# Kernel optimization log

Hardware: AMD Instinct MI355X
Metric: run time of the kernel (lower is better)

The kernel has to match this reference:

```python
import jax, jax.numpy as jnp
import numpy as np

HEADS = 16

def setup_inputs() -> dict:
    key = jax.random.key(0)
    ks = jax.random.split(key, 5)
    B, T, D = 2, 2048, 2048
    s = 0.02
    return {
        "x": jax.random.normal(ks[0], (B, T, D), dtype=jnp.float32),
        "Wq": jax.random.normal(ks[1], (D, D), dtype=jnp.float32) * s,
        "Wk": jax.random.normal(ks[2], (D, D), dtype=jnp.float32) * s,
        "Wv": jax.random.normal(ks[3], (D, D), dtype=jnp.float32) * s,
        "Wo": jax.random.normal(ks[4], (D, D), dtype=jnp.float32) * s,
    }

def reference(x, Wq, Wk, Wv, Wo):
    B, T, _ = x.shape
    H = HEADS
    Dh = Wq.shape[1] // H
    # projections: [B,T,H,Dh]
    q = (x @ Wq).reshape(B, T, H, Dh)
    k = (x @ Wk).reshape(B, T, H, Dh)
    v = (x @ Wv).reshape(B, T, H, Dh)
    # raw scores [B,H,T,T]
    scores = jnp.einsum("bthd,bshd->bhts", q, k)
    # NOTE (faithful to source): mask is multiplicative 0/1 tril (the
    # masked_fill(-inf) in the torch code is not in-place and has no effect),
    # and the scale is sqrt(token_len), not sqrt(head_dim).
    mask = jnp.tril(jnp.ones((T, T), dtype=scores.dtype))
    scores = scores * mask
    attn = jax.nn.softmax(scores / (T ** 0.5), axis=-1)
    out = jnp.einsum("bhts,bshd->bthd", attn, v).reshape(B, T, H * Dh)
    return out @ Wo
```

## Files before the change

### kernel.cpp

```cpp
#include <hip/hip_runtime.h>


typedef __attribute__((ext_vector_type(4))) float  f32x4;
typedef __attribute__((ext_vector_type(8))) short  bf16x8;
typedef __attribute__((ext_vector_type(4))) unsigned short u16x4;

#define AS1 __attribute__((address_space(1)))
#define AS3 __attribute__((address_space(3)))

__device__ __forceinline__ void llds16(const void* g, void* l) {
  __builtin_amdgcn_global_load_lds((const AS1 void*)g, (AS3 void*)l, 16, 0, 0);
}

__device__ __forceinline__ unsigned short f2bf(float f) {
  unsigned int u = __builtin_bit_cast(unsigned int, f);
  u += 0x7fffu + ((u >> 16) & 1u);
  return (unsigned short)(u >> 16);
}

__device__ __forceinline__ unsigned short f2bfru(float f) {
  return (unsigned short)((__builtin_bit_cast(unsigned int, f) + 0x8000u) >> 16);
}

__device__ __forceinline__ float bf2f(unsigned short u) {
  return __builtin_bit_cast(float, (unsigned int)u << 16);
}

__global__ __launch_bounds__(256) void cast_x_kernel(const float* __restrict__ in,
                                                     unsigned short* __restrict__ out) {
  int i = blockIdx.x * 256 + threadIdx.x;
  f32x4 v = ((const f32x4*)in)[i];
  u16x4 o;
  o[0] = f2bf(v[0]); o[1] = f2bf(v[1]); o[2] = f2bf(v[2]); o[3] = f2bf(v[3]);
  ((u16x4*)out)[i] = o;
}

__global__ __launch_bounds__(256) void transpose_w4_kernel(
    const float* __restrict__ W0, const float* __restrict__ W1,
    const float* __restrict__ W2, const float* __restrict__ W3,
    unsigned short* __restrict__ T0, unsigned short* __restrict__ T1,
    unsigned short* __restrict__ T2, unsigned short* __restrict__ T3) {
  __shared__ float tile[32][33];
  const int z = blockIdx.z;
  const float* W = (z == 0) ? W0 : (z == 1) ? W1 : (z == 2) ? W2 : W3;
  unsigned short* Wt = (z == 0) ? T0 : (z == 1) ? T1 : (z == 2) ? T2 : T3;
  const int bx = blockIdx.x << 5;
  const int by = blockIdx.y << 5;
  const int tx = threadIdx.x;
  const int ty = threadIdx.y;
#pragma unroll
  for (int r = ty; r < 32; r += 8)
    tile[r][tx] = W[(size_t)(bx + r) * 2048 + by + tx];
  __syncthreads();
#pragma unroll
  for (int r = ty; r < 32; r += 8)
    Wt[(size_t)(by + r) * 2048 + bx + tx] = f2bf(tile[tx][r]);
}

__global__ __launch_bounds__(512, 2) void gemm_qkv(const unsigned short* __restrict__ A,
                                                   const unsigned short* __restrict__ Bt,
                                                   unsigned short* __restrict__ Qb,
                                                   unsigned short* __restrict__ Kb,
                                                   unsigned short* __restrict__ Vt) {
  constexpr int SLOT = 49152;
  __shared__ __align__(16) char smem[3 * SLOT];
  const int tid  = threadIdx.x;
  const int lane = tid & 63;
  const int w    = tid >> 6;
  const int wr   = w >> 2;
  const int wc   = w & 3;
  const int q16  = lane >> 4;
  const int l15  = lane & 15;
  const int f    = blockIdx.x;
  const int g    = f >> 3;
  const int bn   = (f & 7) * 3 + (g % 3);
  const int bm   = g / 3;

  const int srow = tid >> 3;
  const int scl  = (tid & 7) ^ (srow & 7);
  const unsigned short* aS = A  + (size_t)((bm << 7) + srow) * 2048 + (scl << 3);
  const unsigned short* bS = Bt + (size_t)(bn * 256 + srow) * 2048 + (scl << 3);
  const int sdst = tid << 4;

  const int swzb = (q16 ^ (l15 & 7)) << 4;
  const int aRd  = ((wr << 6) + l15) << 7;
  const int bRd  = 16384 + ((wc << 6) + l15) << 7 == 0 ? 0 : 16384 + (((wc << 6) + l15) << 7);

  f32x4 acc[4][4];
#pragma unroll
  for (int i = 0; i < 4; ++i)
#pragma unroll
    for (int j = 0; j < 4; ++j) acc[i][j] = (f32x4){0.f, 0.f, 0.f, 0.f};

  auto stageT = [&](int kt, char* sb) {
    const size_t ko = (size_t)kt << 6;
    llds16(aS + ko,              sb + sdst);
    llds16(aS + (64 * 2048) + ko, sb + 8192 + sdst);
#pragma unroll
    for (int r = 0; r < 4; ++r)
      llds16(bS + (size_t)r * (64 * 2048) + ko, sb + 16384 + (r << 13) + sdst);
  };

  auto computeT = [&](const char* base) {
#pragma unroll
    for (int ks = 0; ks < 2; ++ks) {
      const int sw = swzb ^ (ks << 6);
      bf16x8 af[4], bf[4];
#pragma unroll
      for (int mi = 0; mi < 4; ++mi)
        af[mi] = *(const bf16x8*)(base + aRd + (mi << 11) + sw);
#pragma unroll
      for (int ni = 0; ni < 4; ++ni)
        bf[ni] = *(const bf16x8*)(base + 16384 + (((wc << 6) + l15) << 7) + (ni << 11) + sw);
      __builtin_amdgcn_s_setprio(1);
#pragma unroll
      for (int mi = 0; mi < 4; ++mi)
#pragma unroll
        for (int ni = 0; ni < 4; ++ni)
          acc[mi][ni] = __builtin_amdgcn_mfma_f32_16x16x32_bf16(af[mi], bf[ni], acc[mi][ni], 0, 0, 0);
      __builtin_amdgcn_s_setprio(0);
    }
  };

  char* s0 = smem;
  char* s1 = smem + SLOT;
  char* s2 = smem + 2 * SLOT;

#define W6()  asm volatile("s_waitcnt vmcnt(6)" ::: "memory")
#define W0()  asm volatile("s_waitcnt vmcnt(0)" ::: "memory")
#define BAR() __builtin_amdgcn_s_barrier()

  stageT(0, s0); stageT(1, s1);
  W6(); BAR();
  stageT(2, s2);
  computeT(s0);
#pragma unroll 1
  for (int b = 1; b <= 25; b += 3) {
    W6(); BAR(); stageT(b + 2, s0); computeT(s1);
    W6(); BAR(); stageT(b + 3, s1); computeT(s2);
    W6(); BAR(); stageT(b + 4, s2); computeT(s0);
  }
  W6(); BAR(); stageT(30, s0); computeT(s1);
  W6(); BAR(); stageT(31, s1); computeT(s2);
  W6(); BAR(); computeT(s0);
  W0(); BAR(); computeT(s1);

#undef W6
#undef W0
#undef BAR

  const float qscale = 0.02209708691207961f;
  const int rb = q16 << 2;
#pragma unroll
  for (int mi = 0; mi < 4; ++mi) {
    int m0 = (bm << 7) + (wr << 6) + (mi << 4) + rb;
#pragma unroll
    for (int ni = 0; ni < 4; ++ni) {
      int gn = (bn << 8) + (wc << 6) + (ni << 4) + l15;
      int region = gn >> 11;
      int nloc = gn & 2047;
      if (region == 0) {
#pragma unroll
        for (int j = 0; j < 4; ++j)
          Qb[(size_t)(m0 + j) * 2048 + nloc] = f2bf(acc[mi][ni][j] * qscale);
      } else if (region == 1) {
#pragma unroll
        for (int j = 0; j < 4; ++j)
          Kb[(size_t)(m0 + j) * 2048 + nloc] = f2bf(acc[mi][ni][j]);
      } else {
        u16x4 pk;
#pragma unroll
        for (int j = 0; j < 4; ++j) pk[j] = f2bf(acc[mi][ni][j]);
        int b = m0 >> 11, t = m0 & 2047;
        *(u16x4*)(Vt + ((size_t)((b << 4) + (nloc >> 7)) * 128 + (nloc & 127)) * 2048 + t) = pk;
      }
    }
  }
}

__global__ __launch_bounds__(256, 2) void gemm_wo(const unsigned short* __restrict__ A,
                                                  const unsigned short* __restrict__ Bt,
                                                  float* __restrict__ Co) {
  constexpr int SLOT = 8192 + 8192;
  __shared__ __align__(16) char smem[3 * SLOT];

  const int tid  = threadIdx.x;
  const int lane = tid & 63;
  const int w    = tid >> 6;
  const int q16  = lane >> 4;
  const int l15  = lane & 15;
  const int f    = blockIdx.x;
  const int g    = f >> 3;
  const int bn   = ((f & 7) << 1) + (g & 1);
  const int bm   = g >> 1;
  const int wmb  = (w >> 1) << 6;
  const int wnb  = (w & 1) << 6;

  f32x4 acc[4][4];
#pragma unroll
  for (int i = 0; i < 4; ++i)
#pragma unroll
    for (int j = 0; j < 4; ++j) acc[i][j] = (f32x4){0.f, 0.f, 0.f, 0.f};

  const int rowA = tid >> 2;
  const int chA  = tid & 3;
  auto stageT = [&](int t, char* sb) {
    const int k0 = t << 5;
#pragma unroll
    for (int r = 0; r < 2; ++r) {
      int row = (r << 6) + rowA;
      const unsigned short* src = A + (size_t)((bm << 7) + row) * 2048 + k0
                                    + ((chA ^ ((row >> 1) & 3)) << 3);
      llds16(src, sb + (r << 12) + (w << 10));
    }
#pragma unroll
    for (int r = 0; r < 2; ++r) {
      int row = (r << 6) + rowA;
      const unsigned short* src = Bt + (size_t)((bn << 7) + row) * 2048 + k0
                                     + ((chA ^ ((row >> 1) & 3)) << 3);
      llds16(src, sb + 8192 + (r << 12) + (w << 10));
    }
  };

  auto computeT = [&](const char* base) {
    bf16x8 af[4], bf[4];
#pragma unroll
    for (int mi = 0; mi < 4; ++mi) {
      int row = wmb + (mi << 4) + l15;
      af[mi] = *(const bf16x8*)(base + (row << 6) + ((q16 ^ ((row >> 1) & 3)) << 4));
    }
#pragma unroll
    for (int ni = 0; ni < 4; ++ni) {
      int row = wnb + (ni << 4) + l15;
      bf[ni] = *(const bf16x8*)(base + 8192 + (row << 6) + ((q16 ^ ((row >> 1) & 3)) << 4));
    }
    __builtin_amdgcn_s_setprio(1);
#pragma unroll
    for (int mi = 0; mi < 4; ++mi)
#pragma unroll
      for (int ni = 0; ni < 4; ++ni)
        acc[mi][ni] = __builtin_amdgcn_mfma_f32_16x16x32_bf16(af[mi], bf[ni], acc[mi][ni], 0, 0, 0);
    __builtin_amdgcn_s_setprio(0);
  };

  auto STEP = [&](int t, char* cbase, char* sbase) {
    asm volatile("s_waitcnt vmcnt(4)" ::: "memory");
    __builtin_amdgcn_s_barrier();
    stageT(t + 2, sbase);
    computeT(cbase);
  };

  char* s0 = smem;
  char* s1 = smem + SLOT;
  char* s2 = smem + 2 * SLOT;

  stageT(0, s0); stageT(1, s1);
#pragma unroll 1
  for (int t = 0; t < 60; t += 3) {
    STEP(t,     s0, s2);
    STEP(t + 1, s1, s0);
    STEP(t + 2, s2, s1);
  }
  STEP(60, s0, s2);
  STEP(61, s1, s0);
  asm volatile("s_waitcnt vmcnt(4)" ::: "memory");
  __builtin_amdgcn_s_barrier();
  computeT(s2);
  asm volatile("s_waitcnt vmcnt(0)" ::: "memory");
  __builtin_amdgcn_s_barrier();
  computeT(s0);

  const int rb = q16 << 2;
#pragma unroll
  for (int mi = 0; mi < 4; ++mi) {
    int m0 = (bm << 7) + wmb + (mi << 4) + rb;
#pragma unroll
    for (int ni = 0; ni < 4; ++ni) {
      int n = (bn << 7) + wnb + (ni << 4) + l15;
#pragma unroll
      for (int j = 0; j < 4; ++j)
        Co[(size_t)(m0 + j) * 2048 + n] = acc[mi][ni][j];
    }
  }
}

__global__ __launch_bounds__(256) void vsuf_kernel(const unsigned short* __restrict__ Vt,
                                                   float* __restrict__ Suf) {
  const int row  = blockIdx.x * 4 + (threadIdx.x >> 6);
  const int lane = threadIdx.x & 63;
  const unsigned short* vp = Vt + (size_t)row * 2048 + (lane << 5);
  float a = 0.f;
#pragma unroll
  for (int c = 0; c < 4; ++c) {
    bf16x8 v = *(const bf16x8*)(vp + (c << 3));
#pragma unroll
    for (int j = 0; j < 8; ++j) a += bf2f((unsigned short)v[j]);
  }
  float I = a;
#pragma unroll
  for (int off = 1; off < 64; off <<= 1) {
    float t = __shfl_down(I, off, 64);
    I += (lane + off < 64) ? t : 0.f;
  }
  Suf[(size_t)lane * 4096 + row] = I;
  if (lane == 0) Suf[(size_t)64 * 4096 + row] = 0.f;
}

__global__ __launch_bounds__(256) void attn_kernel(const unsigned short* __restrict__ Q,
                                                   const unsigned short* __restrict__ K,
                                                   const unsigned short* __restrict__ V,
                                                   const float* __restrict__ Suf,
                                                   unsigned short* __restrict__ O) {
  __shared__ __align__(16) char smem[36864];
  const int tid  = threadIdx.x;
  const int lane = tid & 63;
  const int w    = tid >> 6;
  const int q16  = lane >> 4;
  const int l15  = lane & 15;
  const int f    = blockIdx.x;
  const int bh    = ((f & 7) << 2) + ((f >> 3) & 3);
  const int strip = 31 - (f >> 5);
  const int b  = bh >> 4;
  const size_t qkbase = ((size_t)(b << 11)) * 2048 + ((size_t)(bh & 15) << 7);
  const size_t vbase  = (size_t)bh << 18;
  const int rb = q16 << 2;
  char* Psm = smem + 32768 + (w << 10);

  const int numIter = 2 * strip + 2;
  const int t0 = (strip << 6) + (w << 4);

  auto stage = [&](int s0, int kb, int vb) {
#pragma unroll
    for (int c = 0; c < 2; ++c) {
      int ch = (w << 1) + c;
      int rowK = (ch << 2) + q16;
      int colbK = (l15 << 4) ^ ((rowK & 7) << 4);
      llds16(K + qkbase + (size_t)(s0 + rowK) * 2048 + (colbK >> 1), smem + kb + (ch << 10));
      int rowV = (ch << 4) + (lane >> 2);
      int colbV = ((lane & 3) << 4) ^ (((rowV >> 2) & 3) << 4);
      llds16(V + vbase + (size_t)rowV * 2048 + s0 + (colbV >> 1), smem + vb + (ch << 10));
    }
  };

  bf16x8 qf[4];
  {
    const unsigned short* qp = Q + qkbase + (size_t)(t0 + l15) * 2048 + (q16 << 3);
#pragma unroll
    for (int kk = 0; kk < 4; ++kk) qf[kk] = *(const bf16x8*)(qp + (kk << 5));
  }

  f32x4 oacc[8];
#pragma unroll
  for (int i = 0; i < 8; ++i) oacc[i] = (f32x4){0.f, 0.f, 0.f, 0.f};
  float ell[4] = {0.f, 0.f, 0.f, 0.f};

  stage(0, 0, 16384);
  asm volatile("s_waitcnt vmcnt(0)" ::: "memory");
  __syncthreads();

  int cur = 0;
  for (int it = 0; it < numIter; ++it) {
    const int s0 = it << 5;
    if (it + 1 < numIter)
      stage(s0 + 32, (cur ^ 1) << 13, 16384 + ((cur ^ 1) << 13));

    if (s0 <= t0) {
      const int kb = cur << 13;
      const int vb = 16384 + (cur << 13);

      f32x4 sA = (f32x4){0.f, 0.f, 0.f, 0.f}, sB = (f32x4){0.f, 0.f, 0.f, 0.f};
#pragma unroll
      for (int kk = 0; kk < 4; ++kk) {
        int r0 = l15;
        bf16x8 k0f = *(const bf16x8*)(smem + kb + (r0 << 8) + (((kk << 6) + (q16 << 4)) ^ ((r0 & 7) << 4)));
        sA = __builtin_amdgcn_mfma_f32_16x16x32_bf16(qf[kk], k0f, sA, 0, 0, 0);
        int r1 = 16 + l15;
        bf16x8 k1f = *(const bf16x8*)(smem + kb + (r1 << 8) + (((kk << 6) + (q16 << 4)) ^ ((r1 & 7) << 4)));
        sB = __builtin_amdgcn_mfma_f32_16x16x32_bf16(qf[kk], k1f, sB, 0, 0, 0);
      }

      float pA[4], pB[4];
      if (s0 + 31 <= t0) {
#pragma unroll
        for (int j = 0; j < 4; ++j) {
          pA[j] = __expf(sA[j]);
          pB[j] = __expf(sB[j]);
          ell[j] += pA[j] + pB[j];
        }
      } else {
#pragma unroll
        for (int j = 0; j < 4; ++j) {
          int t  = t0 + rb + j;
          int sa = s0 + l15;
          float vA = (sa <= t)      ? sA[j] : 0.f;
          float vB = (sa + 16 <= t) ? sB[j] : 0.f;
          pA[j] = __expf(vA);
          pB[j] = __expf(vB);
          ell[j] += pA[j] + pB[j];
        }
      }

#pragma unroll
      for (int j = 0; j < 4; ++j) {
        int r   = rb + j;
        int swz = ((r >> 1) & 3) << 4;
        *(unsigned short*)(Psm + (r << 6) + ((l15 << 1) ^ swz))        = f2bfru(pA[j]);
        *(unsigned short*)(Psm + (r << 6) + ((32 + (l15 << 1)) ^ swz)) = f2bfru(pB[j]);
      }
      asm volatile("s_waitcnt lgkmcnt(0)" ::: "memory");

      bf16x8 pa;
      {
        int r = l15;
        pa = *(const bf16x8*)(Psm + (r << 6) + ((q16 << 4) ^ (((r >> 1) & 3) << 4)));
      }
#pragma unroll
      for (int ni = 0; ni < 8; ++ni) {
        int dr = (ni << 4) + l15;
        bf16x8 vbf = *(const bf16x8*)(smem + vb + (dr << 6) + ((q16 << 4) ^ (((dr >> 2) & 3) << 4)));
        oacc[ni] = __builtin_amdgcn_mfma_f32_16x16x32_bf16(pa, vbf, oacc[ni], 0, 0, 0);
      }
    }

    asm volatile("s_waitcnt vmcnt(0)" ::: "memory");
    __syncthreads();
    cur ^= 1;
  }

  const int send = (t0 & ~31) + 32;
  const float* sp = Suf + (size_t)(send >> 5) * 4096 + ((size_t)bh << 7);
  const float extra = (float)(2048 - send);
#pragma unroll
  for (int ni = 0; ni < 8; ++ni) {
    float sv = sp[(ni << 4) + l15];
#pragma unroll
    for (int j = 0; j < 4; ++j) oacc[ni][j] += sv;
  }

#pragma unroll
  for (int j = 0; j < 4; ++j) {
    float r = ell[j];
    r += __shfl_xor(r, 1, 64);
    r += __shfl_xor(r, 2, 64);
    r += __shfl_xor(r, 4, 64);
    r += __shfl_xor(r, 8, 64);
    float inv = 1.0f / (r + extra);
    int t = t0 + rb + j;
    unsigned short* op = O + qkbase + (size_t)t * 2048;
#pragma unroll
    for (int ni = 0; ni < 8; ++ni)
      op[(ni << 4) + l15] = f2bf(oacc[ni][j] * inv);
  }
}

extern "C" void kernel_launch(void* const* d_in, const int* in_sizes, int n_in,
                              void* d_out, int out_size, void* d_ws, size_t ws_size,
                              hipStream_t stream) {
  (void)in_sizes; (void)n_in; (void)out_size; (void)ws_size;
  const float* x  = (const float*)d_in[0];
  const float* Wq = (const float*)d_in[1];
  const float* Wk = (const float*)d_in[2];
  const float* Wv = (const float*)d_in[3];
  const float* Wo = (const float*)d_in[4];
  float* out = (float*)d_out;

  char* ws = (char*)d_ws;
  unsigned short* Xb  = (unsigned short*)(ws);
  unsigned short* Wqt = (unsigned short*)(ws + 16777216);
  unsigned short* Wkt = (unsigned short*)(ws + 16777216 + 8388608);
  unsigned short* Wvt = (unsigned short*)(ws + 16777216 + 2 * 8388608);
  unsigned short* Wot = (unsigned short*)(ws + 16777216 + 3 * 8388608);
  unsigned short* Qb  = (unsigned short*)(ws + 50331648);
  unsigned short* Kb  = (unsigned short*)(ws + 67108864);
  unsigned short* Vt  = (unsigned short*)(ws + 83886080);
  unsigned short* Ob  = Xb;
  float*          Suf = (float*)Wqt;

  cast_x_kernel<<<8192, 256, 0, stream>>>(x, Xb);
  {
    dim3 tb(32, 8), tg(64, 64, 4);
    transpose_w4_kernel<<<tg, tb, 0, stream>>>(Wq, Wk, Wv, Wo, Wqt, Wkt, Wvt, Wot);
  }
  gemm_qkv<<<768, 512, 0, stream>>>(Xb, Wqt, Qb, Kb, Vt);

  vsuf_kernel<<<1024, 256, 0, stream>>>(Vt, Suf);

  attn_kernel<<<1024, 256, 0, stream>>>(Qb, Kb, Vt, Suf, Ob);

  gemm_wo<<<512, 256, 0, stream>>>(Ob, Wot, out);
}
```

Measured before the change: 265.7 us.

## Retile QKV GEMM to 128x384 tiles with BK=32 and 512 blocks

Replaces the 128x256 tile, BK=64 QKV projection GEMM with a 128x384 tile and BK=32 K-step, so each warp computes a 64x96 sub-tile (4x6 MFMA accumulators). The grid drops from 768 to 512 blocks, which fits exactly two waves of 256 CUs at two blocks per CU. Each block reuses its A loads across more output columns and uses less LDS per stage. The cost is twice as many K iterations and barriers, plus more accumulator registers per thread.

```diff
diff --git a/kernel.cpp b/kernel.cpp
--- a/kernel.cpp
+++ b/kernel.cpp
@@ -57,12 +57,12 @@
     Wt[(size_t)(by + r) * 2048 + bx + tx] = f2bf(tile[tx][r]);
 }
 
-__global__ __launch_bounds__(512, 2) void gemm_qkv(const unsigned short* __restrict__ A,
-                                                   const unsigned short* __restrict__ Bt,
-                                                   unsigned short* __restrict__ Qb,
-                                                   unsigned short* __restrict__ Kb,
-                                                   unsigned short* __restrict__ Vt) {
-  constexpr int SLOT = 49152;
+__global__ __launch_bounds__(512, 2) void gemm_qkv2(const unsigned short* __restrict__ A,
+                                                    const unsigned short* __restrict__ Bt,
+                                                    unsigned short* __restrict__ Qb,
+                                                    unsigned short* __restrict__ Kb,
+                                                    unsigned short* __restrict__ Vt) {
+  constexpr int SLOT = 32768;
   __shared__ __align__(16) char smem[3 * SLOT];
   const int tid  = threadIdx.x;
   const int lane = tid & 63;
@@ -72,81 +72,73 @@
   const int q16  = lane >> 4;
   const int l15  = lane & 15;
   const int f    = blockIdx.x;
-  const int g    = f >> 3;
-  const int bn   = (f & 7) * 3 + (g % 3);
-  const int bm   = g / 3;
-
-  const int srow = tid >> 3;
-  const int scl  = (tid & 7) ^ (srow & 7);
+  const int bn   = ((f & 7) << 1) + ((f >> 3) & 1);
+  const int bm   = f >> 4;
+
+  const int srow = tid >> 2;
+  const int scl  = (tid & 3) ^ ((srow >> 1) & 3);
   const unsigned short* aS = A  + (size_t)((bm << 7) + srow) * 2048 + (scl << 3);
-  const unsigned short* bS = Bt + (size_t)(bn * 256 + srow) * 2048 + (scl << 3);
+  const unsigned short* bS = Bt + (size_t)(bn * 384 + srow) * 2048 + (scl << 3);
   const int sdst = tid << 4;
 
-  const int swzb = (q16 ^ (l15 & 7)) << 4;
-  const int aRd  = ((wr << 6) + l15) << 7;
-  const int bRd  = 16384 + ((wc << 6) + l15) << 7 == 0 ? 0 : 16384 + (((wc << 6) + l15) << 7);
-
-  f32x4 acc[4][4];
+  const int swx   = (q16 ^ ((l15 >> 1) & 3)) << 4;
+  const int aBase = (((wr << 6) + l15) << 6) + swx;
+  const int bBase = 8192 + ((wc * 96 + l15) << 6) + swx;
+
+  f32x4 acc[4][6];
 #pragma unroll
   for (int i = 0; i < 4; ++i)
 #pragma unroll
-    for (int j = 0; j < 4; ++j) acc[i][j] = (f32x4){0.f, 0.f, 0.f, 0.f};
+    for (int j = 0; j < 6; ++j) acc[i][j] = (f32x4){0.f, 0.f, 0.f, 0.f};
 
   auto stageT = [&](int kt, char* sb) {
-    const size_t ko = (size_t)kt << 6;
-    llds16(aS + ko,              sb + sdst);
-    llds16(aS + (64 * 2048) + ko, sb + 8192 + sdst);
-#pragma unroll
-    for (int r = 0; r < 4; ++r)
-      llds16(bS + (size_t)r * (64 * 2048) + ko, sb + 16384 + (r << 13) + sdst);
+    const size_t ko = (size_t)kt << 5;
+    llds16(aS + ko, sb + sdst);
+#pragma unroll
+    for (int r = 0; r < 3; ++r)
+      llds16(bS + (size_t)r * (128 * 2048) + ko, sb + 8192 + (r << 13) + sdst);
   };
 
   auto computeT = [&](const char* base) {
-#pragma unroll
-    for (int ks = 0; ks < 2; ++ks) {
-      const int sw = swzb ^ (ks << 6);
-      bf16x8 af[4], bf[4];
-#pragma unroll
-      for (int mi = 0; mi < 4; ++mi)
-        af[mi] = *(const bf16x8*)(base + aRd + (mi << 11) + sw);
-#pragma unroll
-      for (int ni = 0; ni < 4; ++ni)
-        bf[ni] = *(const bf16x8*)(base + 16384 + (((wc << 6) + l15) << 7) + (ni << 11) + sw);
-      __builtin_amdgcn_s_setprio(1);
-#pragma unroll
-      for (int mi = 0; mi < 4; ++mi)
-#pragma unroll
-        for (int ni = 0; ni < 4; ++ni)
-          acc[mi][ni] = __builtin_amdgcn_mfma_f32_16x16x32_bf16(af[mi], bf[ni], acc[mi][ni], 0, 0, 0);
-      __builtin_amdgcn_s_setprio(0);
-    }
+    bf16x8 af[4], bf[6];
+#pragma unroll
+    for (int mi = 0; mi < 4; ++mi)
+      af[mi] = *(const bf16x8*)(base + aBase + (mi << 10));
+#pragma unroll
+    for (int ni = 0; ni < 6; ++ni)
+      bf[ni] = *(const bf16x8*)(base + bBase + (ni << 10));
+    __builtin_amdgcn_s_setprio(1);
+#pragma unroll
+    for (int mi = 0; mi < 4; ++mi)
+#pragma unroll
+      for (int ni = 0; ni < 6; ++ni)
+        acc[mi][ni] = __builtin_amdgcn_mfma_f32_16x16x32_bf16(af[mi], bf[ni], acc[mi][ni], 0, 0, 0);
+    __builtin_amdgcn_s_setprio(0);
   };
 
   char* s0 = smem;
   char* s1 = smem + SLOT;
   char* s2 = smem + 2 * SLOT;
 
-#define W6()  asm volatile("s_waitcnt vmcnt(6)" ::: "memory")
-#define W0()  asm volatile("s_waitcnt vmcnt(0)" ::: "memory")
+#define W4()  asm volatile("s_waitcnt vmcnt(4)" ::: "memory")
+#define WZ()  asm volatile("s_waitcnt vmcnt(0)" ::: "memory")
 #define BAR() __builtin_amdgcn_s_barrier()
 
   stageT(0, s0); stageT(1, s1);
-  W6(); BAR();
-  stageT(2, s2);
-  computeT(s0);
+  W4(); BAR();
+  stageT(2, s2); computeT(s0);
 #pragma unroll 1
-  for (int b = 1; b <= 25; b += 3) {
-    W6(); BAR(); stageT(b + 2, s0); computeT(s1);
-    W6(); BAR(); stageT(b + 3, s1); computeT(s2);
-    W6(); BAR(); stageT(b + 4, s2); computeT(s0);
-  }
-  W6(); BAR(); stageT(30, s0); computeT(s1);
-  W6(); BAR(); stageT(31, s1); computeT(s2);
-  W6(); BAR(); computeT(s0);
-  W0(); BAR(); computeT(s1);
-
-#undef W6
-#undef W0
+  for (int kt = 1; kt <= 58; kt += 3) {
+    W4(); BAR(); stageT(kt + 2, s0); computeT(s1);
+    W4(); BAR(); stageT(kt + 3, s1); computeT(s2);
+    W4(); BAR(); stageT(kt + 4, s2); computeT(s0);
+  }
+  W4(); BAR(); stageT(63, s0); computeT(s1);
+  W4(); BAR(); computeT(s2);
+  WZ(); BAR(); computeT(s0);
+
+#undef W4
+#undef WZ
 #undef BAR
 
   const float qscale = 0.02209708691207961f;
@@ -155,8 +147,8 @@
   for (int mi = 0; mi < 4; ++mi) {
     int m0 = (bm << 7) + (wr << 6) + (mi << 4) + rb;
 #pragma unroll
-    for (int ni = 0; ni < 4; ++ni) {
-      int gn = (bn << 8) + (wc << 6) + (ni << 4) + l15;
+    for (int ni = 0; ni < 6; ++ni) {
+      int gn = bn * 384 + wc * 96 + (ni << 4) + l15;
       int region = gn >> 11;
       int nloc = gn & 2047;
       if (region == 0) {
@@ -481,7 +473,7 @@
     dim3 tb(32, 8), tg(64, 64, 4);
     transpose_w4_kernel<<<tg, tb, 0, stream>>>(Wq, Wk, Wv, Wo, Wqt, Wkt, Wvt, Wot);
   }
-  gemm_qkv<<<768, 512, 0, stream>>>(Xb, Wqt, Qb, Kb, Vt);
+  gemm_qkv2<<<512, 512, 0, stream>>>(Xb, Wqt, Qb, Kb, Vt);
 
   vsuf_kernel<<<1024, 256, 0, stream>>>(Vt, Suf);
 
```

New measurement: 262.1 us. No clear change (-1.4%).

## Enlarge QKV GEMM tile to 256x256 with double-buffered 8-phase schedule

Applied to the files above, without the earlier changes.

The QKV projection GEMM tile grows from 128x256 to 256x256 per block, which halves the grid to 384 blocks and doubles each wave's accumulator count. The triple-buffered LDS pipeline becomes a double-buffered one using 128KB of LDS. Each k-tile is split into four barrier-separated phases of LDS reads followed by MFMA bursts, so loads interleave with compute across waves. The aim is more operand reuse and less global traffic per FLOP, at the cost of higher register pressure, fewer blocks for load balancing, and more barriers.

```diff
diff --git a/kernel.cpp b/kernel.cpp
--- a/kernel.cpp
+++ b/kernel.cpp
@@ -57,13 +57,12 @@
     Wt[(size_t)(by + r) * 2048 + bx + tx] = f2bf(tile[tx][r]);
 }
 
-__global__ __launch_bounds__(512, 2) void gemm_qkv(const unsigned short* __restrict__ A,
-                                                   const unsigned short* __restrict__ Bt,
-                                                   unsigned short* __restrict__ Qb,
-                                                   unsigned short* __restrict__ Kb,
-                                                   unsigned short* __restrict__ Vt) {
-  constexpr int SLOT = 49152;
-  __shared__ __align__(16) char smem[3 * SLOT];
+__global__ __launch_bounds__(512, 2) void gemm_qkv8p(const unsigned short* __restrict__ A,
+                                                     const unsigned short* __restrict__ Bt,
+                                                     unsigned short* __restrict__ Qb,
+                                                     unsigned short* __restrict__ Kb,
+                                                     unsigned short* __restrict__ Vt) {
+  __shared__ __align__(16) char smem[131072];
   const int tid  = threadIdx.x;
   const int lane = tid & 63;
   const int w    = tid >> 6;
@@ -72,88 +71,119 @@
   const int q16  = lane >> 4;
   const int l15  = lane & 15;
   const int f    = blockIdx.x;
-  const int g    = f >> 3;
-  const int bn   = (f & 7) * 3 + (g % 3);
-  const int bm   = g / 3;
-
-  const int srow = tid >> 3;
-  const int scl  = (tid & 7) ^ (srow & 7);
-  const unsigned short* aS = A  + (size_t)((bm << 7) + srow) * 2048 + (scl << 3);
-  const unsigned short* bS = Bt + (size_t)(bn * 256 + srow) * 2048 + (scl << 3);
+  const int xcd  = f & 7;
+  const int idx  = f >> 3;
+  const int bn   = xcd * 3 + (idx % 3);
+  const int bm   = idx / 3;
+
+  const int t8 = tid >> 3;
+  const int tswz = ((tid & 7) ^ (t8 & 7)) << 3;
+  const unsigned short* aS = A  + (size_t)((bm << 8) + t8) * 2048 + tswz;
+  const unsigned short* bS = Bt + (size_t)((bn << 8) + t8) * 2048 + tswz;
   const int sdst = tid << 4;
 
-  const int swzb = (q16 ^ (l15 & 7)) << 4;
-  const int aRd  = ((wr << 6) + l15) << 7;
-  const int bRd  = 16384 + ((wc << 6) + l15) << 7 == 0 ? 0 : 16384 + (((wc << 6) + l15) << 7);
-
-  f32x4 acc[4][4];
-#pragma unroll
-  for (int i = 0; i < 4; ++i)
+  auto stage = [&](int kt, char* buf) {
+    const size_t ko = (size_t)kt << 6;
+#pragma unroll
+    for (int ro = 0; ro < 4; ++ro)
+      llds16(aS + (size_t)(ro << 6) * 2048 + ko, buf + (ro << 13) + sdst);
+#pragma unroll
+    for (int ro = 0; ro < 4; ++ro)
+      llds16(bS + (size_t)(ro << 6) * 2048 + ko, buf + 32768 + (ro << 13) + sdst);
+  };
+
+  const int c0   = (q16 ^ (l15 & 7)) << 4;
+  const int aRow = ((wr << 7) + l15) << 7;
+  const int bRow = 32768 + (((wc << 6) + l15) << 7);
+
+  f32x4 acc[8][4];
+#pragma unroll
+  for (int i = 0; i < 8; ++i)
 #pragma unroll
     for (int j = 0; j < 4; ++j) acc[i][j] = (f32x4){0.f, 0.f, 0.f, 0.f};
 
-  auto stageT = [&](int kt, char* sb) {
-    const size_t ko = (size_t)kt << 6;
-    llds16(aS + ko,              sb + sdst);
-    llds16(aS + (64 * 2048) + ko, sb + 8192 + sdst);
-#pragma unroll
-    for (int r = 0; r < 4; ++r)
-      llds16(bS + (size_t)r * (64 * 2048) + ko, sb + 16384 + (r << 13) + sdst);
-  };
-
-  auto computeT = [&](const char* base) {
-#pragma unroll
-    for (int ks = 0; ks < 2; ++ks) {
-      const int sw = swzb ^ (ks << 6);
-      bf16x8 af[4], bf[4];
-#pragma unroll
-      for (int mi = 0; mi < 4; ++mi)
-        af[mi] = *(const bf16x8*)(base + aRd + (mi << 11) + sw);
+#define LGKM0() do { asm volatile("s_waitcnt lgkmcnt(0)" ::: "memory"); \
+                     __builtin_amdgcn_sched_barrier(0); } while (0)
+#define BAR()   __builtin_amdgcn_s_barrier()
+
+  stage(0, smem);
+
+#pragma unroll 1
+  for (int kt = 0; kt < 32; ++kt) {
+    char* buf = smem + ((kt & 1) << 16);
+    if (kt < 31) {
+      stage(kt + 1, smem + (((kt + 1) & 1) << 16));
+      asm volatile("s_waitcnt vmcnt(8)" ::: "memory");
+    } else {
+      asm volatile("s_waitcnt vmcnt(0)" ::: "memory");
+    }
+    BAR();
+
+    bf16x8 af[4], ag[4], bf0[4], bf1[4];
+#pragma unroll
+    for (int mi = 0; mi < 4; ++mi)
+      af[mi] = *(const bf16x8*)(buf + aRow + (mi << 11) + c0);
+#pragma unroll
+    for (int ni = 0; ni < 4; ++ni)
+      bf0[ni] = *(const bf16x8*)(buf + bRow + (ni << 11) + c0);
+    BAR(); LGKM0();
+    __builtin_amdgcn_s_setprio(1);
+#pragma unroll
+    for (int mi = 0; mi < 4; ++mi)
 #pragma unroll
       for (int ni = 0; ni < 4; ++ni)
-        bf[ni] = *(const bf16x8*)(base + 16384 + (((wc << 6) + l15) << 7) + (ni << 11) + sw);
-      __builtin_amdgcn_s_setprio(1);
-#pragma unroll
-      for (int mi = 0; mi < 4; ++mi)
-#pragma unroll
-        for (int ni = 0; ni < 4; ++ni)
-          acc[mi][ni] = __builtin_amdgcn_mfma_f32_16x16x32_bf16(af[mi], bf[ni], acc[mi][ni], 0, 0, 0);
-      __builtin_amdgcn_s_setprio(0);
-    }
-  };
-
-  char* s0 = smem;
-  char* s1 = smem + SLOT;
-  char* s2 = smem + 2 * SLOT;
-
-#define W6()  asm volatile("s_waitcnt vmcnt(6)" ::: "memory")
-#define W0()  asm volatile("s_waitcnt vmcnt(0)" ::: "memory")
-#define BAR() __builtin_amdgcn_s_barrier()
-
-  stageT(0, s0); stageT(1, s1);
-  W6(); BAR();
-  stageT(2, s2);
-  computeT(s0);
-#pragma unroll 1
-  for (int b = 1; b <= 25; b += 3) {
-    W6(); BAR(); stageT(b + 2, s0); computeT(s1);
-    W6(); BAR(); stageT(b + 3, s1); computeT(s2);
-    W6(); BAR(); stageT(b + 4, s2); computeT(s0);
-  }
-  W6(); BAR(); stageT(30, s0); computeT(s1);
-  W6(); BAR(); stageT(31, s1); computeT(s2);
-  W6(); BAR(); computeT(s0);
-  W0(); BAR(); computeT(s1);
-
-#undef W6
-#undef W0
+        acc[mi][ni] = __builtin_amdgcn_mfma_f32_16x16x32_bf16(af[mi], bf0[ni], acc[mi][ni], 0, 0, 0);
+    __builtin_amdgcn_s_setprio(0);
+    BAR();
+#pragma unroll
+    for (int mi = 0; mi < 4; ++mi)
+      ag[mi] = *(const bf16x8*)(buf + aRow + ((mi + 4) << 11) + c0);
+    BAR(); LGKM0();
+    __builtin_amdgcn_s_setprio(1);
+#pragma unroll
+    for (int mi = 0; mi < 4; ++mi)
+#pragma unroll
+      for (int ni = 0; ni < 4; ++ni)
+        acc[mi + 4][ni] = __builtin_amdgcn_mfma_f32_16x16x32_bf16(ag[mi], bf0[ni], acc[mi + 4][ni], 0, 0, 0);
+    __builtin_amdgcn_s_setprio(0);
+    BAR();
+#pragma unroll
+    for (int mi = 0; mi < 4; ++mi)
+      af[mi] = *(const bf16x8*)(buf + aRow + (mi << 11) + (c0 ^ 64));
+#pragma unroll
+    for (int ni = 0; ni < 4; ++ni)
+      bf1[ni] = *(const bf16x8*)(buf + bRow + (ni << 11) + (c0 ^ 64));
+    BAR(); LGKM0();
+    __builtin_amdgcn_s_setprio(1);
+#pragma unroll
+    for (int mi = 0; mi < 4; ++mi)
+#pragma unroll
+      for (int ni = 0; ni < 4; ++ni)
+        acc[mi][ni] = __builtin_amdgcn_mfma_f32_16x16x32_bf16(af[mi], bf1[ni], acc[mi][ni], 0, 0, 0);
+    __builtin_amdgcn_s_setprio(0);
+    BAR();
+#pragma unroll
+    for (int mi = 0; mi < 4; ++mi)
+      ag[mi] = *(const bf16x8*)(buf + aRow + ((mi + 4) << 11) + (c0 ^ 64));
+    BAR(); LGKM0();
+    __builtin_amdgcn_s_setprio(1);
+#pragma unroll
+    for (int mi = 0; mi < 4; ++mi)
+#pragma unroll
+      for (int ni = 0; ni < 4; ++ni)
+        acc[mi + 4][ni] = __builtin_amdgcn_mfma_f32_16x16x32_bf16(ag[mi], bf1[ni], acc[mi + 4][ni], 0, 0, 0);
+    __builtin_amdgcn_s_setprio(0);
+    BAR();
+  }
+
+#undef LGKM0
 #undef BAR
 
   const float qscale = 0.02209708691207961f;
   const int rb = q16 << 2;
 #pragma unroll
-  for (int mi = 0; mi < 4; ++mi) {
-    int m0 = (bm << 7) + (wr << 6) + (mi << 4) + rb;
+  for (int mi = 0; mi < 8; ++mi) {
+    int m0 = (bm << 8) + (wr << 7) + (mi << 4) + rb;
 #pragma unroll
     for (int ni = 0; ni < 4; ++ni) {
       int gn = (bn << 8) + (wc << 6) + (ni << 4) + l15;
@@ -481,7 +511,7 @@
     dim3 tb(32, 8), tg(64, 64, 4);
     transpose_w4_kernel<<<tg, tb, 0, stream>>>(Wq, Wk, Wv, Wo, Wqt, Wkt, Wvt, Wot);
   }
-  gemm_qkv<<<768, 512, 0, stream>>>(Xb, Wqt, Qb, Kb, Vt);
+  gemm_qkv8p<<<384, 512, 0, stream>>>(Xb, Wqt, Qb, Kb, Vt);
 
   vsuf_kernel<<<1024, 256, 0, stream>>>(Vt, Suf);
 
```

Result: slower. 283.1 us (+6.5%).

## Double attention query rows per wave to reuse K/V tiles across two query groups

Applied to the files above, without the earlier changes.

Each wave in the attention kernel now handles 32 query rows instead of 16. Each K and V fragment loaded from shared memory feeds two MFMAs, and the grid is halved to 512 blocks. Strips are reassigned in a balanced order that interleaves long and short causal strips, and launch bounds request two blocks per CU. This cuts shared-memory reads and per-KV-tile staging per FLOP, at the cost of more registers and fewer blocks.

```diff
diff --git a/kernel.cpp b/kernel.cpp
--- a/kernel.cpp
+++ b/kernel.cpp
@@ -84,7 +84,6 @@
 
   const int swzb = (q16 ^ (l15 & 7)) << 4;
   const int aRd  = ((wr << 6) + l15) << 7;
-  const int bRd  = 16384 + ((wc << 6) + l15) << 7 == 0 ? 0 : 16384 + (((wc << 6) + l15) << 7);
 
   f32x4 acc[4][4];
 #pragma unroll
@@ -94,7 +93,7 @@
 
   auto stageT = [&](int kt, char* sb) {
     const size_t ko = (size_t)kt << 6;
-    llds16(aS + ko,              sb + sdst);
+    llds16(aS + ko,               sb + sdst);
     llds16(aS + (64 * 2048) + ko, sb + 8192 + sdst);
 #pragma unroll
     for (int r = 0; r < 4; ++r)
@@ -306,28 +305,29 @@
   if (lane == 0) Suf[(size_t)64 * 4096 + row] = 0.f;
 }
 
-__global__ __launch_bounds__(256) void attn_kernel(const unsigned short* __restrict__ Q,
-                                                   const unsigned short* __restrict__ K,
-                                                   const unsigned short* __restrict__ V,
-                                                   const float* __restrict__ Suf,
-                                                   unsigned short* __restrict__ O) {
-  __shared__ __align__(16) char smem[36864];
+__global__ __launch_bounds__(256, 2) void attn_kernel(const unsigned short* __restrict__ Q,
+                                                      const unsigned short* __restrict__ K,
+                                                      const unsigned short* __restrict__ V,
+                                                      const float* __restrict__ Suf,
+                                                      unsigned short* __restrict__ O) {
+  __shared__ __align__(16) char smem[40960];
   const int tid  = threadIdx.x;
   const int lane = tid & 63;
   const int w    = tid >> 6;
   const int q16  = lane >> 4;
   const int l15  = lane & 15;
   const int f    = blockIdx.x;
-  const int bh    = ((f & 7) << 2) + ((f >> 3) & 3);
-  const int strip = 31 - (f >> 5);
+  const int bh   = ((f & 7) << 2) + ((f >> 3) & 3);
+  const int fs   = f >> 5;
+  const int strip = (fs < 8) ? (15 - fs) : (fs - 8);
   const int b  = bh >> 4;
   const size_t qkbase = ((size_t)(b << 11)) * 2048 + ((size_t)(bh & 15) << 7);
   const size_t vbase  = (size_t)bh << 18;
   const int rb = q16 << 2;
-  char* Psm = smem + 32768 + (w << 10);
-
-  const int numIter = 2 * strip + 2;
-  const int t0 = (strip << 6) + (w << 4);
+  char* Psm = smem + 32768 + (w << 11);
+
+  const int numIter = 4 * strip + 4;
+  const int t0 = (strip << 7) + (w << 5);
 
   auto stage = [&](int s0, int kb, int vb) {
 #pragma unroll
@@ -342,17 +342,20 @@
     }
   };
 
-  bf16x8 qf[4];
+  bf16x8 qf[4], qg[4];
   {
     const unsigned short* qp = Q + qkbase + (size_t)(t0 + l15) * 2048 + (q16 << 3);
 #pragma unroll
     for (int kk = 0; kk < 4; ++kk) qf[kk] = *(const bf16x8*)(qp + (kk << 5));
-  }
-
-  f32x4 oacc[8];
-#pragma unroll
-  for (int i = 0; i < 8; ++i) oacc[i] = (f32x4){0.f, 0.f, 0.f, 0.f};
-  float ell[4] = {0.f, 0.f, 0.f, 0.f};
+    const unsigned short* qp2 = qp + (size_t)16 * 2048;
+#pragma unroll
+    for (int kk = 0; kk < 4; ++kk) qg[kk] = *(const bf16x8*)(qp2 + (kk << 5));
+  }
+
+  f32x4 oA[8], oB[8];
+#pragma unroll
+  for (int i = 0; i < 8; ++i) { oA[i] = (f32x4){0.f,0.f,0.f,0.f}; oB[i] = (f32x4){0.f,0.f,0.f,0.f}; }
+  float ellA[4] = {0.f,0.f,0.f,0.f}, ellB[4] = {0.f,0.f,0.f,0.f};
 
   stage(0, 0, 16384);
   asm volatile("s_waitcnt vmcnt(0)" ::: "memory");
@@ -368,57 +371,69 @@
       const int kb = cur << 13;
       const int vb = 16384 + (cur << 13);
 
-      f32x4 sA = (f32x4){0.f, 0.f, 0.f, 0.f}, sB = (f32x4){0.f, 0.f, 0.f, 0.f};
+      f32x4 sA = (f32x4){0.f,0.f,0.f,0.f}, sB = sA, sC = sA, sD = sA;
 #pragma unroll
       for (int kk = 0; kk < 4; ++kk) {
-        int r0 = l15;
+        int r0 = l15, r1 = 16 + l15;
         bf16x8 k0f = *(const bf16x8*)(smem + kb + (r0 << 8) + (((kk << 6) + (q16 << 4)) ^ ((r0 & 7) << 4)));
+        bf16x8 k1f = *(const bf16x8*)(smem + kb + (r1 << 8) + (((kk << 6) + (q16 << 4)) ^ ((r1 & 7) << 4)));
         sA = __builtin_amdgcn_mfma_f32_16x16x32_bf16(qf[kk], k0f, sA, 0, 0, 0);
-        int r1 = 16 + l15;
-        bf16x8 k1f = *(const bf16x8*)(smem + kb + (r1 << 8) + (((kk << 6) + (q16 << 4)) ^ ((r1 & 7) << 4)));
+        sC = __builtin_amdgcn_mfma_f32_16x16x32_bf16(qg[kk], k0f, sC, 0, 0, 0);
         sB = __builtin_amdgcn_mfma_f32_16x16x32_bf16(qf[kk], k1f, sB, 0, 0, 0);
+        sD = __builtin_amdgcn_mfma_f32_16x16x32_bf16(qg[kk], k1f, sD, 0, 0, 0);
       }
 
-      float pA[4], pB[4];
-      if (s0 + 31 <= t0) {
+      float pA[4], pB[4], pC[4], pD[4];
+      if (s0 + 32 <= t0) {
 #pragma unroll
         for (int j = 0; j < 4; ++j) {
-          pA[j] = __expf(sA[j]);
-          pB[j] = __expf(sB[j]);
-          ell[j] += pA[j] + pB[j];
+          pA[j] = __expf(sA[j]); pB[j] = __expf(sB[j]);
+          pC[j] = __expf(sC[j]); pD[j] = __expf(sD[j]);
+          ellA[j] += pA[j] + pB[j];
+          ellB[j] += pC[j] + pD[j];
         }
       } else {
 #pragma unroll
         for (int j = 0; j < 4; ++j) {
-          int t  = t0 + rb + j;
+          int tA = t0 + rb + j, tB = tA + 16;
           int sa = s0 + l15;
-          float vA = (sa <= t)      ? sA[j] : 0.f;
-          float vB = (sa + 16 <= t) ? sB[j] : 0.f;
-          pA[j] = __expf(vA);
-          pB[j] = __expf(vB);
-          ell[j] += pA[j] + pB[j];
+          float vA = (sa <= tA)      ? sA[j] : 0.f;
+          float vB = (sa + 16 <= tA) ? sB[j] : 0.f;
+          float vC = (sa <= tB)      ? sC[j] : 0.f;
+          float vD = (sa + 16 <= tB) ? sD[j] : 0.f;
+          pA[j] = __expf(vA); pB[j] = __expf(vB);
+          pC[j] = __expf(vC); pD[j] = __expf(vD);
+          ellA[j] += pA[j] + pB[j];
+          ellB[j] += pC[j] + pD[j];
         }
       }
 
 #pragma unroll
       for (int j = 0; j < 4; ++j) {
-        int r   = rb + j;
-        int swz = ((r >> 1) & 3) << 4;
-        *(unsigned short*)(Psm + (r << 6) + ((l15 << 1) ^ swz))        = f2bfru(pA[j]);
-        *(unsigned short*)(Psm + (r << 6) + ((32 + (l15 << 1)) ^ swz)) = f2bfru(pB[j]);
+        int rA = rb + j;
+        int swzA = ((rA >> 1) & 3) << 4;
+        *(unsigned short*)(Psm + (rA << 6) + ((l15 << 1) ^ swzA))        = f2bfru(pA[j]);
+        *(unsigned short*)(Psm + (rA << 6) + ((32 + (l15 << 1)) ^ swzA)) = f2bfru(pB[j]);
+        int rB = rA + 16;
+        int swzB = ((rB >> 1) & 3) << 4;
+        *(unsigned short*)(Psm + (rB << 6) + ((l15 << 1) ^ swzB))        = f2bfru(pC[j]);
+        *(unsigned short*)(Psm + (rB << 6) + ((32 + (l15 << 1)) ^ swzB)) = f2bfru(pD[j]);
       }
       asm volatile("s_waitcnt lgkmcnt(0)" ::: "memory");
 
-      bf16x8 pa;
+      bf16x8 paA, paB;
       {
         int r = l15;
-        pa = *(const bf16x8*)(Psm + (r << 6) + ((q16 << 4) ^ (((r >> 1) & 3) << 4)));
+        paA = *(const bf16x8*)(Psm + (r << 6) + ((q16 << 4) ^ (((r >> 1) & 3) << 4)));
+        int r2 = 16 + l15;
+        paB = *(const bf16x8*)(Psm + (r2 << 6) + ((q16 << 4) ^ (((r2 >> 1) & 3) << 4)));
       }
 #pragma unroll
       for (int ni = 0; ni < 8; ++ni) {
         int dr = (ni << 4) + l15;
         bf16x8 vbf = *(const bf16x8*)(smem + vb + (dr << 6) + ((q16 << 4) ^ (((dr >> 2) & 3) << 4)));
-        oacc[ni] = __builtin_amdgcn_mfma_f32_16x16x32_bf16(pa, vbf, oacc[ni], 0, 0, 0);
+        oA[ni] = __builtin_amdgcn_mfma_f32_16x16x32_bf16(paA, vbf, oA[ni], 0, 0, 0);
+        oB[ni] = __builtin_amdgcn_mfma_f32_16x16x32_bf16(paB, vbf, oB[ni], 0, 0, 0);
       }
     }
 
@@ -427,19 +442,19 @@
     cur ^= 1;
   }
 
-  const int send = (t0 & ~31) + 32;
+  const int send = t0 + 32;
   const float* sp = Suf + (size_t)(send >> 5) * 4096 + ((size_t)bh << 7);
   const float extra = (float)(2048 - send);
 #pragma unroll
   for (int ni = 0; ni < 8; ++ni) {
     float sv = sp[(ni << 4) + l15];
 #pragma unroll
-    for (int j = 0; j < 4; ++j) oacc[ni][j] += sv;
+    for (int j = 0; j < 4; ++j) { oA[ni][j] += sv; oB[ni][j] += sv; }
   }
 
 #pragma unroll
   for (int j = 0; j < 4; ++j) {
-    float r = ell[j];
+    float r = ellA[j];
     r += __shfl_xor(r, 1, 64);
     r += __shfl_xor(r, 2, 64);
     r += __shfl_xor(r, 4, 64);
@@ -449,7 +464,18 @@
     unsigned short* op = O + qkbase + (size_t)t * 2048;
 #pragma unroll
     for (int ni = 0; ni < 8; ++ni)
-      op[(ni << 4) + l15] = f2bf(oacc[ni][j] * inv);
+      op[(ni << 4) + l15] = f2bf(oA[ni][j] * inv);
+
+    float r2 = ellB[j];
+    r2 += __shfl_xor(r2, 1, 64);
+    r2 += __shfl_xor(r2, 2, 64);
+    r2 += __shfl_xor(r2, 4, 64);
+    r2 += __shfl_xor(r2, 8, 64);
+    float inv2 = 1.0f / (r2 + extra);
+    unsigned short* op2 = op + (size_t)16 * 2048;
+#pragma unroll
+    for (int ni = 0; ni < 8; ++ni)
+      op2[(ni << 4) + l15] = f2bf(oB[ni][j] * inv2);
   }
 }
 
@@ -485,7 +511,7 @@
 
   vsuf_kernel<<<1024, 256, 0, stream>>>(Vt, Suf);
 
-  attn_kernel<<<1024, 256, 0, stream>>>(Qb, Kb, Vt, Suf, Ob);
+  attn_kernel<<<512, 256, 0, stream>>>(Qb, Kb, Vt, Suf, Ob);
 
   gemm_wo<<<512, 256, 0, stream>>>(Ob, Wot, out);
 }
```

After: 260.2 us. -2.1%, faster.
